# Optimization experiments

Measured on AMD Instinct MI355X. Metric: run time of the kernel, lower is better.

The kernel has to match this reference:

```python
import jax, jax.numpy as jnp
import numpy as np
from jax import lax

B, C_IN, C_OUT, KS, K, FD, L = 32, 128, 256, 9, 8, 64, 4096
PAD = KS // 2


def setup_inputs() -> dict:
    key = jax.random.key(0)
    ks = jax.random.split(key, 8)
    X = jax.random.normal(ks[0], (B, C_IN, L), dtype=jnp.float32)
    Z = jax.random.normal(ks[1], (B, FD), dtype=jnp.float32)
    # z_to_in: Linear(fluct_dim, in_planes), xavier-ish init, zero bias
    z_in_w = jax.random.normal(ks[2], (C_IN, FD), dtype=jnp.float32) * (1.0 / np.sqrt(FD))
    z_in_b = jnp.zeros((C_IN,), dtype=jnp.float32)
    # z_to_w MLP: in_planes -> in_planes//2 -> K
    w1 = jax.random.normal(ks[3], (C_IN // 2, C_IN), dtype=jnp.float32) * (1.0 / np.sqrt(C_IN))
    b1 = jax.random.normal(ks[4], (C_IN // 2,), dtype=jnp.float32) * 0.01
    w2 = jax.random.normal(ks[5], (K, C_IN // 2), dtype=jnp.float32) * (1.0 / np.sqrt(C_IN // 2))
    b2 = jax.random.normal(ks[6], (K,), dtype=jnp.float32) * 0.01
    weight_bank = jax.random.normal(ks[7], (K, C_OUT, C_IN, KS), dtype=jnp.float32) * (1.0 / np.sqrt(C_IN * KS))
    bias_bank = jnp.zeros((K, C_OUT), dtype=jnp.float32)
    return {"X": X, "Z": Z, "z_in_w": z_in_w, "z_in_b": z_in_b,
            "w1": w1, "b1": b1, "w2": w2, "b2": b2,
            "weight_bank": weight_bank, "bias_bank": bias_bank}


def _conv_one(x, w):
    # x: (C_in, L); w: (C_out, C_in, KS) -> (C_out, L)
    y = lax.conv_general_dilated(x[None], w, window_strides=(1,),
                                 padding=[(PAD, PAD)],
                                 dimension_numbers=("NCH", "OIH", "NCH"))
    return y[0]


def reference(X, Z, z_in_w, z_in_b, w1, b1, w2, b2, weight_bank, bias_bank):
    # routing: Z -> in_planes -> MLP -> softmax over K (dropout is inference no-op)
    proj = Z @ z_in_w.T + z_in_b                       # (B, C_in)
    h = jax.nn.relu(proj @ w1.T + b1)                  # (B, C_in//2)
    logits = h @ w2.T + b2                             # (B, K)
    omega = jax.nn.softmax(logits, axis=1)             # (B, K)
    # per-sample mixed kernels and biases
    W_tilde = jnp.einsum("bk,koci->boci", omega, weight_bank)  # (B, C_out, C_in, KS)
    b_tilde = omega @ bias_bank                         # (B, C_out)
    # batched per-sample conv (equiv. of the groups=B conv1d trick)
    Y = jax.vmap(_conv_one)(X, W_tilde)                 # (B, C_out, L)
    return Y + b_tilde[:, :, None]
```

## Files before the change

kernel.cpp:

```cpp
#include <hip/hip_runtime.h>
#include <math.h>

#define B_     32
#define C_INP  128
#define C_OUTP 256
#define KS_    9
#define KK_    8
#define FD_    64
#define LL_    4096
#define PAD_   4

#define LPAD   (LL_ + 2 * PAD_)

typedef unsigned short ushort_t;
typedef short bf16x8 __attribute__((ext_vector_type(8)));
typedef float f32x4 __attribute__((ext_vector_type(4)));

__device__ __forceinline__ ushort_t f2bf(float f) {
    unsigned u = __float_as_uint(f);
    unsigned r = (u + 0x7FFFu + ((u >> 16) & 1u)) >> 16;
    return (ushort_t)r;
}

__device__ __forceinline__ void gload16(const void* g, void* l) {
    __builtin_amdgcn_global_load_lds(
        (const __attribute__((address_space(1))) unsigned int*)g,
        (__attribute__((address_space(3))) unsigned int*)l, 16, 0, 0);
}

__global__ __launch_bounds__(256) void routing_kernel(
    const float* __restrict__ Z, const float* __restrict__ z_in_w,
    const float* __restrict__ z_in_b, const float* __restrict__ w1,
    const float* __restrict__ b1, const float* __restrict__ w2,
    const float* __restrict__ b2, const float* __restrict__ bias_bank,
    float* __restrict__ omega_out, float* __restrict__ btilde_out)
{
    const int b = blockIdx.x;
    const int tid = threadIdx.x;
    __shared__ float s_z[FD_];
    __shared__ float s_proj[C_INP];
    __shared__ float s_h[FD_];
    __shared__ float s_logits[KK_];
    __shared__ float s_omega[KK_];

    if (tid < FD_) s_z[tid] = Z[b * FD_ + tid];
    __syncthreads();

    if (tid < C_INP) {
        float acc = z_in_b[tid];
        const float* w = z_in_w + tid * FD_;
        #pragma unroll 8
        for (int f = 0; f < FD_; ++f) acc = fmaf(w[f], s_z[f], acc);
        s_proj[tid] = acc;
    }
    __syncthreads();

    if (tid < FD_) {
        float acc = b1[tid];
        const float* w = w1 + tid * C_INP;
        #pragma unroll 8
        for (int c = 0; c < C_INP; ++c) acc = fmaf(w[c], s_proj[c], acc);
        s_h[tid] = fmaxf(acc, 0.0f);
    }
    __syncthreads();

    if (tid < KK_) {
        float acc = b2[tid];
        const float* w = w2 + tid * FD_;
        #pragma unroll 8
        for (int j = 0; j < FD_; ++j) acc = fmaf(w[j], s_h[j], acc);
        s_logits[tid] = acc;
    }
    __syncthreads();

    if (tid == 0) {
        float m = s_logits[0];
        #pragma unroll
        for (int k = 1; k < KK_; ++k) m = fmaxf(m, s_logits[k]);
        float e[KK_];
        float s = 0.0f;
        #pragma unroll
        for (int k = 0; k < KK_; ++k) { e[k] = expf(s_logits[k] - m); s += e[k]; }
        const float inv = 1.0f / s;
        #pragma unroll
        for (int k = 0; k < KK_; ++k) s_omega[k] = e[k] * inv;
    }
    __syncthreads();

    if (tid < KK_) omega_out[b * KK_ + tid] = s_omega[tid];

    {
        float acc = 0.0f;
        #pragma unroll
        for (int k = 0; k < KK_; ++k) acc = fmaf(s_omega[k], bias_bank[k * C_OUTP + tid], acc);
        btilde_out[b * C_OUTP + tid] = acc;
    }
}

__global__ __launch_bounds__(256) void mix_kernel(
    const float* __restrict__ bank, const float* __restrict__ omega,
    ushort_t* __restrict__ wt)
{
    __shared__ float s_bank[KK_ * C_INP * KS_];
    __shared__ float s_om[B_ * KK_];

    const int o = blockIdx.x;
    const int tid = threadIdx.x;

    s_om[tid] = omega[tid];
    #pragma unroll
    for (int k = 0; k < KK_; ++k) {
        const float* src = bank + ((size_t)(k * C_OUTP + o)) * (C_INP * KS_);
        for (int i = tid; i < C_INP * KS_; i += 256)
            s_bank[k * (C_INP * KS_) + i] = src[i];
    }
    __syncthreads();

    for (int j = tid; j < KS_ * (C_INP / 2); j += 256) {
        const int t = j >> 6;
        const int c = (j & 63) * 2;
        float v0[KK_], v1[KK_];
        #pragma unroll
        for (int k = 0; k < KK_; ++k) {
            v0[k] = s_bank[k * (C_INP * KS_) + c * KS_ + t];
            v1[k] = s_bank[k * (C_INP * KS_) + (c + 1) * KS_ + t];
        }
        #pragma unroll
        for (int b = 0; b < B_; ++b) {
            float a0 = 0.0f, a1 = 0.0f;
            #pragma unroll
            for (int k = 0; k < KK_; ++k) {
                const float om = s_om[b * KK_ + k];
                a0 = fmaf(om, v0[k], a0);
                a1 = fmaf(om, v1[k], a1);
            }
            const unsigned packed = (unsigned)f2bf(a0) | ((unsigned)f2bf(a1) << 16);
            *(unsigned*)&wt[(((size_t)b * KS_ + t) * C_OUTP + o) * C_INP + c] = packed;
        }
    }
}

__global__ __launch_bounds__(256) void transpose_kernel(
    const float* __restrict__ X, ushort_t* __restrict__ XT)
{
    __shared__ ushort_t s_t[64 * 130];

    const int tid = threadIdx.x;
    const int l0 = blockIdx.x * 64;
    const int b = blockIdx.y;

    const int ll = tid & 63;
    const int cq = tid >> 6;
    const float* xb = X + ((size_t)b * C_INP) * LL_;

    #pragma unroll 4
    for (int r = 0; r < 32; ++r) {
        const int c = r * 4 + cq;
        s_t[ll * 130 + c] = f2bf(xb[(size_t)c * LL_ + l0 + ll]);
    }
    __syncthreads();

    ushort_t* xtb = XT + (size_t)b * LPAD * C_INP;
    for (int it = tid; it < 64 * 64; it += 256) {
        const int row = it >> 6;
        const int p = it & 63;
        const unsigned lo = s_t[row * 130 + p * 2];
        const unsigned hi = s_t[row * 130 + p * 2 + 1];
        *(unsigned*)(xtb + ((size_t)(4 + l0 + row)) * C_INP + p * 2) = lo | (hi << 16);
    }
    if (l0 == 0) {
        const int row = tid >> 6, p = tid & 63;
        *(unsigned*)(xtb + (size_t)row * C_INP + p * 2) = 0u;
    }
    if (l0 == LL_ - 64) {
        const int row = tid >> 6, p = tid & 63;
        *(unsigned*)(xtb + ((size_t)(LL_ + PAD_ + row)) * C_INP + p * 2) = 0u;
    }
}

__global__ __launch_bounds__(512, 2) void gemm_kernel(
    const ushort_t* __restrict__ XT, const ushort_t* __restrict__ WT,
    const float* __restrict__ btilde, float* __restrict__ Y)
{
    __shared__ __align__(16) ushort_t sW[2][256 * 64];
    __shared__ __align__(16) ushort_t sX[2][264 * 64];

    const int tid = threadIdx.x;
    const int wid = tid >> 6;
    const int lane = tid & 63;

    const int wg = blockIdx.x;
    const int logical = (wg & 7) * 64 + (wg >> 3);
    const int b  = logical >> 4;
    const int l0 = (logical & 15) << 8;

    {
        const ushort_t* xtb = XT + ((size_t)b * LPAD + l0) * C_INP;
        #pragma unroll
        for (int g0 = 0; g0 < 4224; g0 += 512) {
            const int g = g0 + tid;
            if (g < 4224) {
                const int ch = g / 2112;
                const int gg = g - ch * 2112;
                const int row = gg >> 3;
                const int pc = gg & 7;
                const int scol = pc ^ (row & 7);
                gload16(xtb + row * C_INP + ch * 64 + scol * 8,
                        &sX[ch][0] + gg * 8);
            }
        }
        const ushort_t* wbase = WT + (((size_t)b * KS_ + 0) * C_OUTP) * C_INP;
        #pragma unroll
        for (int it = 0; it < 4; ++it) {
            const int g = it * 512 + tid;
            const int row = g >> 3;
            const int pc = g & 7;
            const int scol = pc ^ (row & 7);
            gload16(wbase + row * C_INP + scol * 8, &sW[0][0] + g * 8);
        }
    }
    __syncthreads();

    const int ln15 = lane & 15;
    const int lh = lane >> 4;
    const int wm0 = (wid >> 2) * 128;
    const int wn0 = (wid & 3) * 64;

    f32x4 acc[8][4];
    #pragma unroll
    for (int i = 0; i < 8; ++i)
        #pragma unroll
        for (int j = 0; j < 4; ++j) acc[i][j] = (f32x4){0.f, 0.f, 0.f, 0.f};

    #pragma unroll 1
    for (int s = 0; s < 2 * KS_; ++s) {
        const int buf = s & 1;
        const int t = s >> 1;
        const int ch = s & 1;

        if (s < 2 * KS_ - 1) {
            const int s1 = s + 1;
            const int t1 = s1 >> 1;
            const int ch1 = s1 & 1;
            const ushort_t* wbase =
                WT + (((size_t)b * KS_ + t1) * C_OUTP) * C_INP + ch1 * 64;
            #pragma unroll
            for (int it = 0; it < 4; ++it) {
                const int g = it * 512 + tid;
                const int row = g >> 3;
                const int pc = g & 7;
                const int scol = pc ^ (row & 7);
                gload16(wbase + row * C_INP + scol * 8, &sW[buf ^ 1][0] + g * 8);
            }
        }

        const ushort_t* wh = &sW[buf][0];
        const ushort_t* xh = &sX[ch][0];
        #pragma unroll
        for (int kk = 0; kk < 2; ++kk) {
            bf16x8 a[8], bx[4];
            #pragma unroll
            for (int i = 0; i < 8; ++i) {
                const int arow = wm0 + i * 16 + ln15;
                a[i] = *(const bf16x8*)&wh[arow * 64 + (((kk * 4 + lh) ^ (arow & 7)) << 3)];
            }
            #pragma unroll
            for (int j = 0; j < 4; ++j) {
                const int brow = wn0 + t + j * 16 + ln15;
                bx[j] = *(const bf16x8*)&xh[brow * 64 + (((kk * 4 + lh) ^ (brow & 7)) << 3)];
            }
            __builtin_amdgcn_s_setprio(1);
            #pragma unroll
            for (int i = 0; i < 8; ++i)
                #pragma unroll
                for (int j = 0; j < 4; ++j)
                    acc[i][j] = __builtin_amdgcn_mfma_f32_16x16x32_bf16(
                        a[i], bx[j], acc[i][j], 0, 0, 0);
            __builtin_amdgcn_s_setprio(0);
        }
        __syncthreads();
    }

    #pragma unroll
    for (int i = 0; i < 8; ++i) {
        const int obase = wm0 + i * 16 + lh * 4;
        const float4 bt = *(const float4*)&btilde[b * C_OUTP + obase];
        #pragma unroll
        for (int j = 0; j < 4; ++j) {
            const int lcol = l0 + wn0 + j * 16 + ln15;
            float* yp = Y + ((size_t)(b * C_OUTP + obase)) * LL_ + lcol;
            yp[0]           = acc[i][j][0] + bt.x;
            yp[LL_]         = acc[i][j][1] + bt.y;
            yp[2 * LL_]     = acc[i][j][2] + bt.z;
            yp[3 * LL_]     = acc[i][j][3] + bt.w;
        }
    }
}

#define O_TILE 8
#define T_PAD  12
__global__ __launch_bounds__(256) void conv_kernel(
    const float* __restrict__ X, const float* __restrict__ bank,
    const float* __restrict__ omega, const float* __restrict__ btilde,
    float* __restrict__ Y)
{
    __shared__ __align__(16) float s_w[C_INP * O_TILE * T_PAD];
    __shared__ float s_om[KK_];

    const int tid = threadIdx.x;
    const int o_base = blockIdx.x * O_TILE;
    const int b = blockIdx.y;

    if (tid < KK_) s_om[tid] = omega[b * KK_ + tid];
    __syncthreads();

    {
        const size_t kstride = (size_t)C_OUTP * C_INP * KS_;
        const float* bank_base = bank + (size_t)o_base * C_INP * KS_;
        for (int idx = tid; idx < O_TILE * C_INP * KS_; idx += 256) {
            const int o = idx / (C_INP * KS_);
            const int rem = idx - o * (C_INP * KS_);
            const int c = rem / KS_;
            const int t = rem - c * KS_;
            const float* p = bank_base + idx;
            float acc = 0.0f;
            #pragma unroll
            for (int k = 0; k < KK_; ++k) acc = fmaf(s_om[k], p[k * kstride], acc);
            s_w[(c * O_TILE + o) * T_PAD + t] = acc;
        }
    }
    __syncthreads();

    const int og = tid >> 7;
    const int lg = tid & 127;
    const float* xb = X + (size_t)b * C_INP * LL_;

    float bt[4];
    #pragma unroll
    for (int o = 0; o < 4; ++o) bt[o] = btilde[b * C_OUTP + o_base + og * 4 + o];

    for (int it = 0; it < 4; ++it) {
        const int l0 = it * 1024 + lg * 8;
        const int lx = l0 - PAD_;
        const bool fast = (lx >= 0) && (lx + 16 <= LL_);

        float acc[4][8];
        #pragma unroll
        for (int o = 0; o < 4; ++o)
            #pragma unroll
            for (int j = 0; j < 8; ++j) acc[o][j] = 0.0f;

        #pragma unroll 1
        for (int c = 0; c < C_INP; ++c) {
            const float* xrow = xb + (size_t)c * LL_;
            float x[16];
            if (fast) {
                const float4* p = reinterpret_cast<const float4*>(xrow + lx);
                const float4 a0 = p[0], a1 = p[1], a2 = p[2], a3 = p[3];
                x[0]=a0.x; x[1]=a0.y; x[2]=a0.z; x[3]=a0.w;
                x[4]=a1.x; x[5]=a1.y; x[6]=a1.z; x[7]=a1.w;
                x[8]=a2.x; x[9]=a2.y; x[10]=a2.z; x[11]=a2.w;
                x[12]=a3.x; x[13]=a3.y; x[14]=a3.z; x[15]=a3.w;
            } else {
                #pragma unroll
                for (int j = 0; j < 16; ++j) {
                    const int q = lx + j;
                    x[j] = (q >= 0 && q < LL_) ? xrow[q] : 0.0f;
                }
            }
            const float* wp = &s_w[(c * O_TILE + og * 4) * T_PAD];
            #pragma unroll
            for (int o = 0; o < 4; ++o) {
                #pragma unroll
                for (int t = 0; t < KS_; ++t) {
                    const float wv = wp[o * T_PAD + t];
                    #pragma unroll
                    for (int j = 0; j < 8; ++j)
                        acc[o][j] = fmaf(wv, x[j + t], acc[o][j]);
                }
            }
        }

        float* yb = Y + ((size_t)(b * C_OUTP + o_base + og * 4)) * LL_ + l0;
        #pragma unroll
        for (int o = 0; o < 4; ++o) {
            float4 r0, r1;
            r0.x = acc[o][0] + bt[o]; r0.y = acc[o][1] + bt[o];
            r0.z = acc[o][2] + bt[o]; r0.w = acc[o][3] + bt[o];
            r1.x = acc[o][4] + bt[o]; r1.y = acc[o][5] + bt[o];
            r1.z = acc[o][6] + bt[o]; r1.w = acc[o][7] + bt[o];
            float4* yp = reinterpret_cast<float4*>(yb + (size_t)o * LL_);
            yp[0] = r0; yp[1] = r1;
        }
    }
}

extern "C" void kernel_launch(void* const* d_in, const int* in_sizes, int n_in,
                              void* d_out, int out_size, void* d_ws, size_t ws_size,
                              hipStream_t stream)
{
    const float* X         = (const float*)d_in[0];
    const float* Z         = (const float*)d_in[1];
    const float* z_in_w    = (const float*)d_in[2];
    const float* z_in_b    = (const float*)d_in[3];
    const float* w1        = (const float*)d_in[4];
    const float* b1        = (const float*)d_in[5];
    const float* w2        = (const float*)d_in[6];
    const float* b2        = (const float*)d_in[7];
    const float* bank      = (const float*)d_in[8];
    const float* bias_bank = (const float*)d_in[9];
    float* out = (float*)d_out;

    char* ws = (char*)d_ws;
    float* omega  = (float*)ws;
    float* btilde = (float*)(ws + 1024);
    ushort_t* wt  = (ushort_t*)(ws + 1024 + 32768);
    ushort_t* XT  = (ushort_t*)(ws + 1024 + 32768 + (size_t)B_ * KS_ * C_OUTP * C_INP * 2);
    const size_t WS_NEEDED = 1024 + 32768
        + (size_t)B_ * KS_ * C_OUTP * C_INP * 2
        + (size_t)B_ * LPAD * C_INP * 2;

    routing_kernel<<<B_, 256, 0, stream>>>(Z, z_in_w, z_in_b, w1, b1, w2, b2,
                                           bias_bank, omega, btilde);

    if (ws_size >= WS_NEEDED) {
        mix_kernel<<<C_OUTP, 256, 0, stream>>>(bank, omega, wt);
        transpose_kernel<<<dim3(LL_ / 64, B_), 256, 0, stream>>>(X, XT);
        gemm_kernel<<<512, 512, 0, stream>>>(XT, wt, btilde, out);
    } else {
        dim3 grid(C_OUTP / O_TILE, B_);
        conv_kernel<<<grid, 256, 0, stream>>>(X, bank, omega, btilde, out);
    }
}
```

Measured before the change: 137.1 us.

## Restructure weight staging into a 4-slot, 3-deep async ring with split-phase barriers

The conv-as-GEMM kernel now streams weight tiles in 32-wide K chunks through a four-slot LDS ring with three stages in flight. It issues each prefetch in two halves interleaved with two MFMA phases and uses raw s_barrier plus explicit vmcnt waits in place of a full __syncthreads per step. The X tile is stored as one 128-channel swizzled block instead of two 64-channel halves. The aim is to hide global-to-LDS latency and cut barrier stalls, at the cost of more fine-grained iterations and fragile manual waitcnt ordering.

New measurement: 131.2 us. -4.3%, faster.

```diff
diff --git a/kernel.cpp b/kernel.cpp
--- a/kernel.cpp
+++ b/kernel.cpp
@@ -182,8 +182,8 @@
     const ushort_t* __restrict__ XT, const ushort_t* __restrict__ WT,
     const float* __restrict__ btilde, float* __restrict__ Y)
 {
-    __shared__ __align__(16) ushort_t sW[2][256 * 64];
-    __shared__ __align__(16) ushort_t sX[2][264 * 64];
+    __shared__ __align__(16) ushort_t sX[264 * 128];
+    __shared__ __align__(16) ushort_t sWr[4][256 * 32];
 
     const int tid = threadIdx.x;
     const int wid = tid >> 6;
@@ -194,29 +194,22 @@
     const int b  = logical >> 4;
     const int l0 = (logical & 15) << 8;
 
-    {
-        const ushort_t* xtb = XT + ((size_t)b * LPAD + l0) * C_INP;
-        #pragma unroll
-        for (int g0 = 0; g0 < 4224; g0 += 512) {
-            const int g = g0 + tid;
-            if (g < 4224) {
-                const int ch = g / 2112;
-                const int gg = g - ch * 2112;
-                const int row = gg >> 3;
-                const int pc = gg & 7;
-                const int scol = pc ^ (row & 7);
-                gload16(xtb + row * C_INP + ch * 64 + scol * 8,
-                        &sX[ch][0] + gg * 8);
-            }
-        }
-        const ushort_t* wbase = WT + (((size_t)b * KS_ + 0) * C_OUTP) * C_INP;
-        #pragma unroll
-        for (int it = 0; it < 4; ++it) {
-            const int g = it * 512 + tid;
-            const int row = g >> 3;
-            const int pc = g & 7;
-            const int scol = pc ^ (row & 7);
-            gload16(wbase + row * C_INP + scol * 8, &sW[0][0] + g * 8);
+    const ushort_t* xtb = XT + ((size_t)b * LPAD + l0) * C_INP;
+    const ushort_t* wtb = WT + (size_t)b * KS_ * C_OUTP * C_INP;
+
+    for (int g = tid; g < 4224; g += 512) {
+        const int row = g >> 4;
+        const int pcp = g & 15;
+        gload16(xtb + row * C_INP + ((pcp ^ (row & 7)) * 8), sX + g * 8);
+    }
+    #pragma unroll
+    for (int p = 0; p < 3; ++p) {
+        ushort_t* wd = sWr[p];
+        const ushort_t* wsp = wtb + p * 32;
+        #pragma unroll
+        for (int itr = 0; itr < 2; ++itr) {
+            const int g = itr * 512 + tid;
+            gload16(wsp + (g >> 2) * C_INP + (g & 3) * 8, wd + g * 8);
         }
     }
     __syncthreads();
@@ -233,53 +226,67 @@
         for (int j = 0; j < 4; ++j) acc[i][j] = (f32x4){0.f, 0.f, 0.f, 0.f};
 
     #pragma unroll 1
-    for (int s = 0; s < 2 * KS_; ++s) {
-        const int buf = s & 1;
-        const int t = s >> 1;
-        const int ch = s & 1;
-
-        if (s < 2 * KS_ - 1) {
-            const int s1 = s + 1;
-            const int t1 = s1 >> 1;
-            const int ch1 = s1 & 1;
-            const ushort_t* wbase =
-                WT + (((size_t)b * KS_ + t1) * C_OUTP) * C_INP + ch1 * 64;
-            #pragma unroll
-            for (int it = 0; it < 4; ++it) {
-                const int g = it * 512 + tid;
-                const int row = g >> 3;
-                const int pc = g & 7;
-                const int scol = pc ^ (row & 7);
-                gload16(wbase + row * C_INP + scol * 8, &sW[buf ^ 1][0] + g * 8);
-            }
-        }
-
-        const ushort_t* wh = &sW[buf][0];
-        const ushort_t* xh = &sX[ch][0];
-        #pragma unroll
-        for (int kk = 0; kk < 2; ++kk) {
-            bf16x8 a[8], bx[4];
-            #pragma unroll
-            for (int i = 0; i < 8; ++i) {
-                const int arow = wm0 + i * 16 + ln15;
-                a[i] = *(const bf16x8*)&wh[arow * 64 + (((kk * 4 + lh) ^ (arow & 7)) << 3)];
-            }
-            #pragma unroll
-            for (int j = 0; j < 4; ++j) {
-                const int brow = wn0 + t + j * 16 + ln15;
-                bx[j] = *(const bf16x8*)&xh[brow * 64 + (((kk * 4 + lh) ^ (brow & 7)) << 3)];
-            }
-            __builtin_amdgcn_s_setprio(1);
-            #pragma unroll
-            for (int i = 0; i < 8; ++i)
-                #pragma unroll
-                for (int j = 0; j < 4; ++j)
-                    acc[i][j] = __builtin_amdgcn_mfma_f32_16x16x32_bf16(
-                        a[i], bx[j], acc[i][j], 0, 0, 0);
-            __builtin_amdgcn_s_setprio(0);
-        }
-        __syncthreads();
-    }
+    for (int hs = 0; hs < 36; ++hs) {
+        const int t = hs >> 2;
+        const int q = hs & 3;
+        int hs2 = hs + 3; if (hs2 >= 36) hs2 -= 36;
+        const int t2 = hs2 >> 2;
+        const int q2 = hs2 & 3;
+        const ushort_t* wr = sWr[hs & 3];
+        ushort_t* wdst = sWr[hs2 & 3];
+        const ushort_t* wsrc = wtb + ((size_t)t2 * C_OUTP) * C_INP + q2 * 32;
+
+        bf16x8 a[8], bx[4];
+
+        #pragma unroll
+        for (int i = 0; i < 4; ++i) {
+            const int arow = wm0 + i * 16 + ln15;
+            a[i] = *(const bf16x8*)&wr[arow * 32 + lh * 8];
+        }
+        #pragma unroll
+        for (int j = 0; j < 4; ++j) {
+            const int brow = wn0 + t + j * 16 + ln15;
+            const int pcx = (q * 4 + lh) ^ (brow & 7);
+            bx[j] = *(const bf16x8*)&sX[brow * 128 + pcx * 8];
+        }
+        {
+            const int g = tid;
+            gload16(wsrc + (g >> 2) * C_INP + (g & 3) * 8, wdst + g * 8);
+        }
+        __builtin_amdgcn_s_barrier();
+        __builtin_amdgcn_s_setprio(1);
+        #pragma unroll
+        for (int i = 0; i < 4; ++i)
+            #pragma unroll
+            for (int j = 0; j < 4; ++j)
+                acc[i][j] = __builtin_amdgcn_mfma_f32_16x16x32_bf16(
+                    a[i], bx[j], acc[i][j], 0, 0, 0);
+        __builtin_amdgcn_s_setprio(0);
+
+        #pragma unroll
+        for (int i = 4; i < 8; ++i) {
+            const int arow = wm0 + i * 16 + ln15;
+            a[i] = *(const bf16x8*)&wr[arow * 32 + lh * 8];
+        }
+        {
+            const int g = 512 + tid;
+            gload16(wsrc + (g >> 2) * C_INP + (g & 3) * 8, wdst + g * 8);
+        }
+        __builtin_amdgcn_s_barrier();
+        __builtin_amdgcn_s_setprio(1);
+        #pragma unroll
+        for (int i = 4; i < 8; ++i)
+            #pragma unroll
+            for (int j = 0; j < 4; ++j)
+                acc[i][j] = __builtin_amdgcn_mfma_f32_16x16x32_bf16(
+                    a[i], bx[j], acc[i][j], 0, 0, 0);
+        __builtin_amdgcn_s_setprio(0);
+
+        asm volatile("s_waitcnt vmcnt(4)" ::: "memory");
+        __builtin_amdgcn_s_barrier();
+        __builtin_amdgcn_sched_barrier(0);
+    }
+    asm volatile("s_waitcnt vmcnt(0)" ::: "memory");
 
     #pragma unroll
     for (int i = 0; i < 8; ++i) {
```
